# Optimization experiments

Hardware: AMD Instinct MI355X
Metric: run time of the kernel (lower is better)

Reference implementation:

```python
import jax, jax.numpy as jnp
import numpy as np
from jax.scipy.special import logsumexp

B, T, D = 256, 2048, 64


def setup_inputs() -> dict:
    key = jax.random.key(0)
    k1, k2, k3, k4 = jax.random.split(key, 4)
    p = jax.random.normal(k1, (B, T, D), dtype=jnp.float32)
    labels = jax.random.randint(k2, (B, T), 0, D)
    y = jax.nn.one_hot(labels, D, dtype=jnp.int32)  # [B,T,D] one-hot labels
    # valid lengths in [T//2, T]; mask == 1 marks padding positions
    lengths = jax.random.randint(k3, (B,), T // 2, T + 1)
    mask = (jnp.arange(T)[None, :] >= lengths[:, None]).astype(jnp.int32)
    transition = 0.1 * jax.random.normal(k4, (D, D), dtype=jnp.float32)
    return {"p": p, "y": y, "mask": mask, "transition": transition}


def reference(p, y, mask, transition):
    # CRF negative log-likelihood per example: logZ - emission_score - transition_score
    Bb = p.shape[0]
    valid = (1 - mask).astype(jnp.float32)            # [B,T], 1 = valid token
    y1 = y.astype(jnp.float32) * valid[:, :, None]    # masked one-hot labels
    s1 = jnp.sum(y1 * p, axis=(1, 2))                 # emission score
    pair = jnp.einsum('btd,bte->bde', y1[:, :-1], y1[:, 1:])  # label bigram counts
    s2 = jnp.sum(pair * transition, axis=(1, 2))      # transition score

    # forward algorithm: alpha_t = p_t + logsumexp(alpha_{t-1}[:, :, None] + T)
    def step(state, inp):
        new = inp + logsumexp(state[:, :, None] + transition[None, :, :], axis=1)
        return new, new

    xs = jnp.moveaxis(p[:, 1:, :], 1, 0)              # [T-1, B, D]
    _, a1 = jax.lax.scan(step, p[:, 0, :], xs)        # a1: [T-1, B, D]

    # index of alpha at the last valid timestep (length L -> a1 index L-2)
    m1 = jnp.argmin(
        jnp.concatenate([valid.astype(jnp.int32), jnp.zeros((Bb, 1), jnp.int32)], axis=1),
        axis=1) - 2                                   # [B]
    last = a1[m1, jnp.arange(Bb)]                     # [B, D]
    logZ = logsumexp(last, axis=-1)
    return logZ - s1 - s2
```

## Files before the change

kernel.cpp:

```cpp
#include <hip/hip_runtime.h>
#include <stdint.h>
#include <string.h>

#define BB 256
#define TT 2048
#define DD 64
#define CC 64
#define SS 32
#define C_L2E 1.44269504f
#define C_LN2 0.69314718f
#define C_BIAS 0.0028174f

typedef short sh8  __attribute__((ext_vector_type(8)));
typedef float f32x4 __attribute__((ext_vector_type(4)));

union BU { sh8 v8; unsigned int u[4]; unsigned short s[8]; };

__device__ __forceinline__ float expf_fast(float x) { return __builtin_amdgcn_exp2f(x * C_L2E); }
__device__ __forceinline__ unsigned short bf16rne(float x) {
    unsigned int u = __float_as_uint(x);
    u += 0x7FFF + ((u >> 16) & 1u);
    return (unsigned short)(u >> 16);
}
__device__ __forceinline__ unsigned int pkbf(float hi, float lo) {
    return __builtin_amdgcn_perm(__float_as_uint(hi), __float_as_uint(lo), 0x07060302u);
}

#define DPPMAX(x, ctrl, rm, bm) { int _xi = __float_as_int(x);                              \
    int _yi = __builtin_amdgcn_update_dpp(_xi, _xi, ctrl, rm, bm, false);                   \
    x = fmaxf(x, __int_as_float(_yi)); }

__global__ __launch_bounds__(256) void crf_score(
    const float* __restrict__ p, const int* __restrict__ y,
    const int* __restrict__ mask, const float* __restrict__ tr,
    float* __restrict__ wsS, int* __restrict__ wsL)
{
    __shared__ int mk[257];
    __shared__ unsigned char labs[257];
    __shared__ float redf[4];
    __shared__ int redi[4];
    const int c = blockIdx.y, t0 = blockIdx.x * 256;
    const int tid = threadIdx.x;
    const int g = tid & 15, sub = tid >> 4;
    const size_t cb = (size_t)c * TT;

    mk[tid] = mask[cb + t0 + tid];
    if (tid == 0) mk[256] = (t0 + 256 < TT) ? mask[cb + t0 + 256] : 1;
    __syncthreads();

    float s1 = 0.f;
    int vc = 0;
#pragma unroll
    for (int k = 0; k < 16; ++k) {
        const int ti = k * 16 + sub;
        if (mk[ti] == 0) {
            int4 v = ((const int4*)y)[(cb + t0 + ti) * 16 + g];
            int cand = v.w ? 4 * g + 3 : v.z ? 4 * g + 2 : v.y ? 4 * g + 1 : v.x ? 4 * g : -1;
#pragma unroll
            for (int xm = 1; xm <= 8; xm <<= 1) {
                int o = __shfl_xor(cand, xm, 16);
                cand = o > cand ? o : cand;
            }
            if (g == 0) {
                labs[ti] = (unsigned char)cand;
                s1 += p[(cb + t0 + ti) * DD + cand];
                vc += 1;
            }
        }
    }
    if (tid < 16 && mk[256] == 0) {
        int4 v = ((const int4*)y)[(cb + t0 + 256) * 16 + tid];
        int cand = v.w ? 4 * tid + 3 : v.z ? 4 * tid + 2 : v.y ? 4 * tid + 1 : v.x ? 4 * tid : -1;
#pragma unroll
        for (int xm = 1; xm <= 8; xm <<= 1) {
            int o = __shfl_xor(cand, xm, 16);
            cand = o > cand ? o : cand;
        }
        if (tid == 0) labs[256] = (unsigned char)cand;
    }
    __syncthreads();

    float s2 = 0.f;
    if (mk[tid + 1] == 0)
        s2 = tr[(int)labs[tid] * DD + (int)labs[tid + 1]];

    float acc = s1 + s2;
#pragma unroll
    for (int xm = 32; xm >= 1; xm >>= 1) { acc += __shfl_xor(acc, xm, 64); vc += __shfl_xor(vc, xm, 64); }
    if ((tid & 63) == 0) { redf[tid >> 6] = acc; redi[tid >> 6] = vc; }
    __syncthreads();
    if (tid == 0) {
        atomicAdd(&wsS[c], redf[0] + redf[1] + redf[2] + redf[3]);
        atomicAdd(&wsL[c], redi[0] + redi[1] + redi[2] + redi[3]);
    }
}

__global__ __launch_bounds__(256) void crf_probe(
    const float* __restrict__ p, const float* __restrict__ tr,
    const int* __restrict__ wsL,
    unsigned short* __restrict__ wsA, unsigned short* __restrict__ wsB, int* __restrict__ wsSig)
{
    const int tid = threadIdx.x, w = tid >> 6, lane = tid & 63;
    const int q = lane >> 4, ml = lane & 15;
    const int cg = blockIdx.x;
    const int ic = blockIdx.y * 2 + (w >> 1);
    const int bwd = w & 1;
    const int c = cg * 16 + ml;
    const int Lml = wsL[c];
    const int t0 = ic * SS, t1 = t0 + SS;
    const int ts = (ic == 0) ? 1 : t0;
    const float* prow = p + (size_t)c * TT * DD;

    BU A[4][2];
#pragma unroll
    for (int mt = 0; mt < 4; ++mt)
#pragma unroll
        for (int kt2 = 0; kt2 < 2; ++kt2)
#pragma unroll
            for (int j = 0; j < 8; ++j) {
                int lam = 32 * kt2 + 16 * (j >> 2) + 4 * q + (j & 3);
                float tv = bwd ? tr[(16 * mt + ml) * DD + lam] : tr[lam * DD + 16 * mt + ml];
                A[mt][kt2].s[j] = (short)bf16rne(expf_fast(tv));
            }

    float xs[16];
    if (!bwd && ic == 0) {
#pragma unroll
        for (int k = 0; k < 4; ++k) {
            f32x4 v = *(const f32x4*)(prow + 16 * k + 4 * q);
#pragma unroll
            for (int r = 0; r < 4; ++r)
                xs[(k >> 1) * 8 + (k & 1) * 4 + r] = __builtin_amdgcn_exp2f(fmaf(v[r], C_L2E, C_BIAS));
        }
    } else {
#pragma unroll
        for (int i = 0; i < 16; ++i) xs[i] = 1.0f;
    }

    int mL = Lml;
#pragma unroll
    for (int xm = 32; xm >= 1; xm >>= 1) { int o = __shfl_xor(mL, xm, 64); mL = o > mL ? o : mL; }
    int ibeg = 0, iend = SS;
    if (!bwd) { int ir = mL - t0; if (ir < 0) ir = 0; iend = (ir + 3) & ~3; if (iend > SS) iend = SS; }
    else      { int ir = t1 - mL; if (ir < 0) ir = 0; ibeg = ir & ~3; if (ibeg > SS) ibeg = SS; }

    int sig = 0;
    const f32x4 z4 = {0.f, 0.f, 0.f, 0.f};

    if (ibeg < iend) {
        f32x4 er[4][4];
#pragma unroll
        for (int s = 0; s < 4; ++s) {
            int i = ibeg + s;
            int t = bwd ? (t1 - 1 - i) : (t0 + i);
#pragma unroll
            for (int k = 0; k < 4; ++k)
                er[s][k] = *(const f32x4*)(prow + (size_t)t * DD + 16 * k + 4 * q);
        }
        for (int ib = ibeg; ib < iend; ib += 4) {
#pragma unroll
            for (int s = 0; s < 4; ++s) {
                const int i = ib + s;
                const int t = bwd ? (t1 - 1 - i) : (t0 + i);
                const bool act = (t >= ts) && (t < Lml);
                float ee[4][4];
#pragma unroll
                for (int k = 0; k < 4; ++k)
#pragma unroll
                    for (int r = 0; r < 4; ++r)
                        ee[k][r] = __builtin_amdgcn_exp2f(fmaf(er[s][k][r], C_L2E, C_BIAS));
                {
                    int ipf = i + 4;
                    int tpf = bwd ? (t1 - 1 - ipf) : (t0 + ipf);
                    if (tpf < t0) tpf = t0;
                    if (tpf > t1 - 1) tpf = t1 - 1;
#pragma unroll
                    for (int k = 0; k < 4; ++k)
                        er[s][k] = *(const f32x4*)(prow + (size_t)tpf * DD + 16 * k + 4 * q);
                }
                float cand[16];
                BU Bf[2];
                f32x4 acc[4];
                if (!bwd) {
#pragma unroll
                    for (int kt2 = 0; kt2 < 2; ++kt2)
#pragma unroll
                        for (int jj = 0; jj < 4; ++jj)
                            Bf[kt2].u[jj] = pkbf(xs[kt2 * 8 + 2 * jj + 1], xs[kt2 * 8 + 2 * jj]);
#pragma unroll
                    for (int mt = 0; mt < 4; ++mt) {
                        acc[mt] = __builtin_amdgcn_mfma_f32_16x16x32_bf16(A[mt][0].v8, Bf[0].v8, z4, 0, 0, 0);
                        acc[mt] = __builtin_amdgcn_mfma_f32_16x16x32_bf16(A[mt][1].v8, Bf[1].v8, acc[mt], 0, 0, 0);
                    }
#pragma unroll
                    for (int mt = 0; mt < 4; ++mt)
#pragma unroll
                        for (int r = 0; r < 4; ++r)
                            cand[(mt >> 1) * 8 + (mt & 1) * 4 + r] = acc[mt][r] * ee[mt][r];
                } else {
                    float xsc[16];
#pragma unroll
                    for (int kt2 = 0; kt2 < 2; ++kt2)
#pragma unroll
                        for (int h = 0; h < 2; ++h)
#pragma unroll
                            for (int r = 0; r < 4; ++r)
                                xsc[kt2 * 8 + h * 4 + r] = xs[kt2 * 8 + h * 4 + r] * ee[2 * kt2 + h][r];
#pragma unroll
                    for (int kt2 = 0; kt2 < 2; ++kt2)
#pragma unroll
                        for (int jj = 0; jj < 4; ++jj)
                            Bf[kt2].u[jj] = pkbf(xsc[kt2 * 8 + 2 * jj + 1], xsc[kt2 * 8 + 2 * jj]);
#pragma unroll
                    for (int mt = 0; mt < 4; ++mt) {
                        acc[mt] = __builtin_amdgcn_mfma_f32_16x16x32_bf16(A[mt][0].v8, Bf[0].v8, z4, 0, 0, 0);
                        acc[mt] = __builtin_amdgcn_mfma_f32_16x16x32_bf16(A[mt][1].v8, Bf[1].v8, acc[mt], 0, 0, 0);
                    }
#pragma unroll
                    for (int mt = 0; mt < 4; ++mt)
#pragma unroll
                        for (int r = 0; r < 4; ++r)
                            cand[(mt >> 1) * 8 + (mt & 1) * 4 + r] = acc[mt][r];
                }
                if (s == 3) {
                    float mx = fabsf(cand[0]);
#pragma unroll
                    for (int i2 = 1; i2 < 16; ++i2) mx = fmaxf(mx, fabsf(cand[i2]));
                    DPPMAX(mx, 0x111, 0xF, 0xF); DPPMAX(mx, 0x112, 0xF, 0xF);
                    DPPMAX(mx, 0x114, 0xF, 0xF); DPPMAX(mx, 0x118, 0xF, 0xF);
                    DPPMAX(mx, 0x142, 0xA, 0xF); DPPMAX(mx, 0x143, 0xC, 0xF);
                    int smx = __builtin_amdgcn_readlane(__float_as_int(mx), 63);
                    int kk = ((smx >> 23) & 255) - 127;
                    kk = kk < -124 ? -124 : (kk > 124 ? 124 : kk);
                    float sc = __int_as_float((unsigned)(127 - kk) << 23);
#pragma unroll
                    for (int i2 = 0; i2 < 16; ++i2) cand[i2] *= sc;
                    if (act) sig += kk;
                }
#pragma unroll
                for (int i2 = 0; i2 < 16; ++i2) xs[i2] = act ? cand[i2] : xs[i2];
            }
        }
    }

    unsigned short* dst = (bwd ? wsB : wsA) + ((size_t)c * CC + ic) * 64;
#pragma unroll
    for (int kt2 = 0; kt2 < 2; ++kt2)
#pragma unroll
        for (int h = 0; h < 2; ++h)
#pragma unroll
            for (int r = 0; r < 4; ++r)
                dst[32 * kt2 + 16 * h + 4 * q + r] = bf16rne(xs[kt2 * 8 + h * 4 + r]);
    if (!bwd && q == 0) wsSig[c * CC + ic] = sig;
}

__global__ __launch_bounds__(256) void crf_combine(
    const unsigned short* __restrict__ wsA, const unsigned short* __restrict__ wsB,
    const int* __restrict__ wsSig, const float* __restrict__ wsS,
    float* __restrict__ out)
{
    __shared__ float eParts[4];
    const int tid = threadIdx.x, w = tid >> 6, lane = tid & 63;
    const int c = blockIdx.x;

    float Ep = 0.f;
#pragma unroll
    for (int k = 0; k < 16; ++k) {
        const int i = w * 16 + k;
        if (i == 0) continue;
        float b  = __uint_as_float((unsigned)wsB[((size_t)c * CC + i) * 64 + lane] << 16);
        float ap = __uint_as_float((unsigned)wsA[((size_t)c * CC + i - 1) * 64 + lane] << 16);
        float d1 = b * ap, d0 = b;
#pragma unroll
        for (int xm = 32; xm >= 1; xm >>= 1) { d1 += __shfl_xor(d1, xm, 64); d0 += __shfl_xor(d0, xm, 64); }
        Ep += (float)wsSig[c * CC + i] + __builtin_amdgcn_logf(d1) - __builtin_amdgcn_logf(d0);
    }
    if (w == 0) Ep += (float)wsSig[c * CC];
    if (w == 3) {
        float al = __uint_as_float((unsigned)wsA[((size_t)c * CC + CC - 1) * 64 + lane] << 16);
#pragma unroll
        for (int xm = 32; xm >= 1; xm >>= 1) al += __shfl_xor(al, xm, 64);
        Ep += __builtin_amdgcn_logf(al);
    }
    if (lane == 0) eParts[w] = Ep;
    __syncthreads();
    if (tid == 0) {
        float E = eParts[0] + eParts[1] + eParts[2] + eParts[3];
        out[c] = C_LN2 * E - wsS[c];
    }
}

extern "C" void kernel_launch(void* const* d_in, const int* in_sizes, int n_in,
                              void* d_out, int out_size, void* d_ws, size_t ws_size,
                              hipStream_t stream) {
    const float* p  = (const float*)d_in[0];
    const int*   y  = (const int*)d_in[1];
    const int*   mk = (const int*)d_in[2];
    const float* tr = (const float*)d_in[3];
    float* out = (float*)d_out;

    float* wsS  = (float*)d_ws;
    int*   wsL  = (int*)((char*)d_ws + 1024);
    int*   wsSg = (int*)((char*)d_ws + 2048);
    unsigned short* wsA = (unsigned short*)((char*)d_ws + 131072);
    unsigned short* wsB = (unsigned short*)((char*)d_ws + 131072 + (2u << 20));

    hipMemsetAsync(d_ws, 0, 2048, stream);
    crf_score<<<dim3(8, BB), dim3(256), 0, stream>>>(p, y, mk, tr, wsS, wsL);
    crf_probe<<<dim3(16, CC / 2), dim3(256), 0, stream>>>(p, tr, wsL, wsA, wsB, wsSg);
    crf_combine<<<dim3(BB), dim3(256), 0, stream>>>(wsA, wsB, wsSg, wsS, out);
}
```

Before: 317.5 us.

## Double time chunks, precompute transition fragments, drop atomics and memset

The time axis is split into 128 chunks of 16 steps instead of 64 chunks of 32, which doubles the probe grid and halves each wave's serial chain. The combine step now reduces twice as many chunk boundaries. Exp'd bf16 transition MFMA fragments are computed once by a tiny kernel and loaded by every probe wave, instead of each wave recomputing them. The score kernel writes per-block partials instead of using atomics, which removes the memset; it also hoists all label loads ahead of the mask-dependent branch. In exchange it adds one kernel launch and more boundary work in combine.

Result: slower. 328.2 us (+3.4%).

```diff
diff --git a/kernel.cpp b/kernel.cpp
--- a/kernel.cpp
+++ b/kernel.cpp
@@ -5,8 +5,8 @@
 #define BB 256
 #define TT 2048
 #define DD 64
-#define CC 64
-#define SS 32
+#define CC 128
+#define SS 16
 #define C_L2E 1.44269504f
 #define C_LN2 0.69314718f
 #define C_BIAS 0.0028174f
@@ -30,16 +30,37 @@
     int _yi = __builtin_amdgcn_update_dpp(_xi, _xi, ctrl, rm, bm, false);                   \
     x = fmaxf(x, __int_as_float(_yi)); }
 
+__global__ __launch_bounds__(128) void crf_frag(
+    const float* __restrict__ tr, unsigned int* __restrict__ wsF)
+{
+    const int tid = threadIdx.x, bwd = tid >> 6, lane = tid & 63;
+    const int q = lane >> 4, ml = lane & 15;
+#pragma unroll
+    for (int mt = 0; mt < 4; ++mt)
+#pragma unroll
+        for (int kt2 = 0; kt2 < 2; ++kt2) {
+            BU a;
+#pragma unroll
+            for (int j = 0; j < 8; ++j) {
+                int lam = 32 * kt2 + 16 * (j >> 2) + 4 * q + (j & 3);
+                float tv = bwd ? tr[(16 * mt + ml) * DD + lam] : tr[lam * DD + 16 * mt + ml];
+                a.s[j] = (short)bf16rne(expf_fast(tv));
+            }
+            uint4 pk; pk.x = a.u[0]; pk.y = a.u[1]; pk.z = a.u[2]; pk.w = a.u[3];
+            *(uint4*)(wsF + ((size_t)(bwd * 8 + mt * 2 + kt2) * 64 + lane) * 4) = pk;
+        }
+}
+
 __global__ __launch_bounds__(256) void crf_score(
     const float* __restrict__ p, const int* __restrict__ y,
     const int* __restrict__ mask, const float* __restrict__ tr,
-    float* __restrict__ wsS, int* __restrict__ wsL)
+    float* __restrict__ wsS8, int* __restrict__ wsL8)
 {
     __shared__ int mk[257];
     __shared__ unsigned char labs[257];
     __shared__ float redf[4];
     __shared__ int redi[4];
-    const int c = blockIdx.y, t0 = blockIdx.x * 256;
+    const int c = blockIdx.y, bx = blockIdx.x, t0 = bx * 256;
     const int tid = threadIdx.x;
     const int g = tid & 15, sub = tid >> 4;
     const size_t cb = (size_t)c * TT;
@@ -48,29 +69,31 @@
     if (tid == 0) mk[256] = (t0 + 256 < TT) ? mask[cb + t0 + 256] : 1;
     __syncthreads();
 
+    int4 v[16];
+#pragma unroll
+    for (int k = 0; k < 16; ++k)
+        v[k] = ((const int4*)y)[(cb + t0 + k * 16 + sub) * 16 + g];
+
     float s1 = 0.f;
     int vc = 0;
 #pragma unroll
     for (int k = 0; k < 16; ++k) {
         const int ti = k * 16 + sub;
-        if (mk[ti] == 0) {
-            int4 v = ((const int4*)y)[(cb + t0 + ti) * 16 + g];
-            int cand = v.w ? 4 * g + 3 : v.z ? 4 * g + 2 : v.y ? 4 * g + 1 : v.x ? 4 * g : -1;
-#pragma unroll
-            for (int xm = 1; xm <= 8; xm <<= 1) {
-                int o = __shfl_xor(cand, xm, 16);
-                cand = o > cand ? o : cand;
-            }
-            if (g == 0) {
-                labs[ti] = (unsigned char)cand;
-                s1 += p[(cb + t0 + ti) * DD + cand];
-                vc += 1;
-            }
+        int cand = v[k].w ? 4 * g + 3 : v[k].z ? 4 * g + 2 : v[k].y ? 4 * g + 1 : v[k].x ? 4 * g : -1;
+#pragma unroll
+        for (int xm = 1; xm <= 8; xm <<= 1) {
+            int o = __shfl_xor(cand, xm, 16);
+            cand = o > cand ? o : cand;
+        }
+        if (g == 0 && mk[ti] == 0) {
+            labs[ti] = (unsigned char)cand;
+            s1 += p[(cb + t0 + ti) * DD + cand];
+            vc += 1;
         }
     }
     if (tid < 16 && mk[256] == 0) {
-        int4 v = ((const int4*)y)[(cb + t0 + 256) * 16 + tid];
-        int cand = v.w ? 4 * tid + 3 : v.z ? 4 * tid + 2 : v.y ? 4 * tid + 1 : v.x ? 4 * tid : -1;
+        int4 vb = ((const int4*)y)[(cb + t0 + 256) * 16 + tid];
+        int cand = vb.w ? 4 * tid + 3 : vb.z ? 4 * tid + 2 : vb.y ? 4 * tid + 1 : vb.x ? 4 * tid : -1;
 #pragma unroll
         for (int xm = 1; xm <= 8; xm <<= 1) {
             int o = __shfl_xor(cand, xm, 16);
@@ -90,14 +113,14 @@
     if ((tid & 63) == 0) { redf[tid >> 6] = acc; redi[tid >> 6] = vc; }
     __syncthreads();
     if (tid == 0) {
-        atomicAdd(&wsS[c], redf[0] + redf[1] + redf[2] + redf[3]);
-        atomicAdd(&wsL[c], redi[0] + redi[1] + redi[2] + redi[3]);
+        wsS8[c * 8 + bx] = redf[0] + redf[1] + redf[2] + redf[3];
+        wsL8[c * 8 + bx] = redi[0] + redi[1] + redi[2] + redi[3];
     }
 }
 
 __global__ __launch_bounds__(256) void crf_probe(
-    const float* __restrict__ p, const float* __restrict__ tr,
-    const int* __restrict__ wsL,
+    const float* __restrict__ p, const unsigned int* __restrict__ wsF,
+    const int* __restrict__ wsL8,
     unsigned short* __restrict__ wsA, unsigned short* __restrict__ wsB, int* __restrict__ wsSig)
 {
     const int tid = threadIdx.x, w = tid >> 6, lane = tid & 63;
@@ -106,22 +129,25 @@
     const int ic = blockIdx.y * 2 + (w >> 1);
     const int bwd = w & 1;
     const int c = cg * 16 + ml;
-    const int Lml = wsL[c];
     const int t0 = ic * SS, t1 = t0 + SS;
     const int ts = (ic == 0) ? 1 : t0;
     const float* prow = p + (size_t)c * TT * DD;
 
+    int Lml;
+    {
+        const int4* lp = (const int4*)(wsL8 + c * 8);
+        int4 a0 = lp[0], a1 = lp[1];
+        Lml = a0.x + a0.y + a0.z + a0.w + a1.x + a1.y + a1.z + a1.w;
+    }
+
     BU A[4][2];
 #pragma unroll
     for (int mt = 0; mt < 4; ++mt)
 #pragma unroll
-        for (int kt2 = 0; kt2 < 2; ++kt2)
-#pragma unroll
-            for (int j = 0; j < 8; ++j) {
-                int lam = 32 * kt2 + 16 * (j >> 2) + 4 * q + (j & 3);
-                float tv = bwd ? tr[(16 * mt + ml) * DD + lam] : tr[lam * DD + 16 * mt + ml];
-                A[mt][kt2].s[j] = (short)bf16rne(expf_fast(tv));
-            }
+        for (int kt2 = 0; kt2 < 2; ++kt2) {
+            uint4 pk = *(const uint4*)(wsF + ((size_t)(bwd * 8 + mt * 2 + kt2) * 64 + lane) * 4);
+            A[mt][kt2].u[0] = pk.x; A[mt][kt2].u[1] = pk.y; A[mt][kt2].u[2] = pk.z; A[mt][kt2].u[3] = pk.w;
+        }
 
     float xs[16];
     if (!bwd && ic == 0) {
@@ -256,7 +282,7 @@
 
 __global__ __launch_bounds__(256) void crf_combine(
     const unsigned short* __restrict__ wsA, const unsigned short* __restrict__ wsB,
-    const int* __restrict__ wsSig, const float* __restrict__ wsS,
+    const int* __restrict__ wsSig, const float* __restrict__ wsS8,
     float* __restrict__ out)
 {
     __shared__ float eParts[4];
@@ -265,8 +291,8 @@
 
     float Ep = 0.f;
 #pragma unroll
-    for (int k = 0; k < 16; ++k) {
-        const int i = w * 16 + k;
+    for (int k = 0; k < 32; ++k) {
+        const int i = w * 32 + k;
         if (i == 0) continue;
         float b  = __uint_as_float((unsigned)wsB[((size_t)c * CC + i) * 64 + lane] << 16);
         float ap = __uint_as_float((unsigned)wsA[((size_t)c * CC + i - 1) * 64 + lane] << 16);
@@ -286,7 +312,10 @@
     __syncthreads();
     if (tid == 0) {
         float E = eParts[0] + eParts[1] + eParts[2] + eParts[3];
-        out[c] = C_LN2 * E - wsS[c];
+        const float4* sp = (const float4*)(wsS8 + c * 8);
+        float4 s0 = sp[0], s1 = sp[1];
+        float S = (s0.x + s0.y + s0.z + s0.w) + (s1.x + s1.y + s1.z + s1.w);
+        out[c] = C_LN2 * E - S;
     }
 }
 
@@ -299,14 +328,15 @@
     const float* tr = (const float*)d_in[3];
     float* out = (float*)d_out;
 
-    float* wsS  = (float*)d_ws;
-    int*   wsL  = (int*)((char*)d_ws + 1024);
-    int*   wsSg = (int*)((char*)d_ws + 2048);
-    unsigned short* wsA = (unsigned short*)((char*)d_ws + 131072);
-    unsigned short* wsB = (unsigned short*)((char*)d_ws + 131072 + (2u << 20));
-
-    hipMemsetAsync(d_ws, 0, 2048, stream);
-    crf_score<<<dim3(8, BB), dim3(256), 0, stream>>>(p, y, mk, tr, wsS, wsL);
-    crf_probe<<<dim3(16, CC / 2), dim3(256), 0, stream>>>(p, tr, wsL, wsA, wsB, wsSg);
-    crf_combine<<<dim3(BB), dim3(256), 0, stream>>>(wsA, wsB, wsSg, wsS, out);
-}
+    float* wsS8 = (float*)d_ws;
+    int*   wsL8 = (int*)((char*)d_ws + 8192);
+    unsigned int* wsF = (unsigned int*)((char*)d_ws + 16384);
+    int*   wsSg = (int*)((char*)d_ws + 32768);
+    unsigned short* wsA = (unsigned short*)((char*)d_ws + 163840);
+    unsigned short* wsB = (unsigned short*)((char*)d_ws + 163840 + (4u << 20));
+
+    crf_frag<<<dim3(1), dim3(128), 0, stream>>>(tr, wsF);
+    crf_score<<<dim3(8, BB), dim3(256), 0, stream>>>(p, y, mk, tr, wsS8, wsL8);
+    crf_probe<<<dim3(16, CC / 2), dim3(256), 0, stream>>>(p, wsF, wsL8, wsA, wsB, wsSg);
+    crf_combine<<<dim3(BB), dim3(256), 0, stream>>>(wsA, wsB, wsSg, wsS8, out);
+}
```
